# Performance work log

Measured on AMD Instinct MI355X. Metric: run time of the kernel, lower is better.

The kernel has to match this reference:

```python
import jax, jax.numpy as jnp
import numpy as np

LEVEL = 8
THRESHOLD = 0.1
INV_SQRT2 = 0.7071067811865476  # 1/sqrt(2), db1 (Haar) filter coefficient

# Static frequency-order permutation: pywt get_level(order='freq') places the
# natural-order (path-lex: aa,ad,da,dd,...) node n at frequency position gray(n).
_g = np.arange(2 ** LEVEL)
_FREQ_PERM = np.argsort(_g ^ (_g >> 1))  # freq[j] = natural[_FREQ_PERM[j]]


def setup_inputs() -> dict:
    key = jax.random.key(0)
    x = jax.random.normal(key, (128, 65536), dtype=jnp.float32)
    return {"x": x}


def _wavelet_packet_leaves(x):
    """Full db1 wavelet-packet tree to LEVEL; returns [B, 2^L, T/2^L] in freq order.

    For Haar with even-length inputs, pywt's symmetric extension is a no-op:
    a[k] = (x[2k]+x[2k+1])/sqrt2, d[k] = (x[2k]-x[2k+1])/sqrt2.
    """
    B, T = x.shape
    c = x[:, None, :]  # [B, nodes=1, len=T]
    for _ in range(LEVEL):
        ev = c[..., 0::2]
        od = c[..., 1::2]
        a = (ev + od) * INV_SQRT2
        d = (ev - od) * INV_SQRT2
        # interleave children (a,d) adjacent -> natural (path-lex) node order
        c = jnp.concatenate([a[:, :, None, :], d[:, :, None, :]], axis=2)
        c = c.reshape(B, -1, a.shape[-1])
    return c[:, _FREQ_PERM, :]


def reference(x):
    coeffs = _wavelet_packet_leaves(x)          # [B, 2^L, n]
    p = coeffs * coeffs
    p = p / (jnp.sum(p, axis=-1, keepdims=True) + 1e-8)
    entropy = -jnp.sum(p * jnp.log(p + 1e-8), axis=-1)  # [B, 2^L]
    keep = entropy > THRESHOLD                           # [B, 2^L] bool
    # Original returns per-batch stacks of kept nodes (variable length);
    # jit-friendly equivalent: zero out pruned nodes and return the mask.
    out = jnp.where(keep[..., None], coeffs, jnp.zeros((), coeffs.dtype))
    return out, entropy, keep
```

## Files before the change

kernel.cpp:

```cpp
#include <hip/hip_runtime.h>

static constexpr int BROWS = 128;
static constexpr int T     = 65536;
static constexpr int CL    = 256;
static constexpr int NCH   = 256;
static constexpr int NODES = 256;
static constexpr int KG    = 32;
static constexpr int LSTR  = 257;

__device__ __forceinline__ int freq_pos(int h) {
    unsigned r = __brev((unsigned)h) >> 24;
    return (int)(r ^ (r >> 1));
}

__global__ __launch_bounds__(256) void wht_kernel(const float* __restrict__ x,
                                                  float* __restrict__ coeffs) {
    __shared__ float lds[KG][LSTR];

    const int b    = blockIdx.x >> 3;
    const int kg   = blockIdx.x & 7;
    const int k0   = kg * KG;
    const int lane = threadIdx.x & 63;
    const int wave = threadIdx.x >> 6;

    const float* xb = x + (size_t)b * T;

    #pragma unroll
    for (int c = 0; c < KG / 4; ++c) {
        const int kl = wave * (KG / 4) + c;
        float4 v = *(const float4*)(xb + (size_t)(k0 + kl) * CL + lane * 4);

        float4 w;
        w.x = v.x + v.y; w.y = v.x - v.y;
        w.z = v.z + v.w; w.w = v.z - v.w;
        v.x = w.x + w.z; v.z = w.x - w.z;
        v.y = w.y + w.w; v.w = w.y - w.w;

        #pragma unroll
        for (int s = 0; s < 6; ++s) {
            const int mask = 1 << s;
            float4 o;
            o.x = __shfl_xor(v.x, mask, 64);
            o.y = __shfl_xor(v.y, mask, 64);
            o.z = __shfl_xor(v.z, mask, 64);
            o.w = __shfl_xor(v.w, mask, 64);
            const float sgn = 1.0f - 2.0f * (float)((lane >> s) & 1);
            v.x = fmaf(sgn, v.x, o.x);
            v.y = fmaf(sgn, v.y, o.y);
            v.z = fmaf(sgn, v.z, o.z);
            v.w = fmaf(sgn, v.w, o.w);
        }

        lds[kl][freq_pos(4 * lane + 0)] = v.x * 0.0625f;
        lds[kl][freq_pos(4 * lane + 1)] = v.y * 0.0625f;
        lds[kl][freq_pos(4 * lane + 2)] = v.z * 0.0625f;
        lds[kl][freq_pos(4 * lane + 3)] = v.w * 0.0625f;
    }
    __syncthreads();

    float* ob = coeffs + (size_t)b * T + k0;
    const int kk = (threadIdx.x & 7) * 4;
    const int m0 = threadIdx.x >> 3;
    #pragma unroll
    for (int p = 0; p < 8; ++p) {
        const int m = p * 32 + m0;
        float4 v;
        v.x = lds[kk + 0][m];
        v.y = lds[kk + 1][m];
        v.z = lds[kk + 2][m];
        v.w = lds[kk + 3][m];
        *(float4*)(ob + (size_t)m * NCH + kk) = v;
    }
}

__global__ __launch_bounds__(256) void entropy_kernel(float* __restrict__ coeffs,
                                                      float* __restrict__ entropy,
                                                      float* __restrict__ keep) {
    const int lane = threadIdx.x & 63;
    const int wave = threadIdx.x >> 6;
    const int row  = blockIdx.x * 4 + wave;

    float* cp = coeffs + (size_t)row * NCH;
    float4 v = *(const float4*)(cp + lane * 4);

    float4 sq;
    sq.x = v.x * v.x; sq.y = v.y * v.y;
    sq.z = v.z * v.z; sq.w = v.w * v.w;

    float s = sq.x + sq.y + sq.z + sq.w;
    #pragma unroll
    for (int m = 1; m < 64; m <<= 1) s += __shfl_xor(s, m, 64);

    const float inv = 1.0f / (s + 1e-8f);
    const float p0 = sq.x * inv, p1 = sq.y * inv, p2 = sq.z * inv, p3 = sq.w * inv;
    float t = p0 * logf(p0 + 1e-8f) + p1 * logf(p1 + 1e-8f)
            + p2 * logf(p2 + 1e-8f) + p3 * logf(p3 + 1e-8f);
    #pragma unroll
    for (int m = 1; m < 64; m <<= 1) t += __shfl_xor(t, m, 64);

    const float e  = -t;
    const bool  kp = e > 0.1f;

    if (!kp) {
        *(float4*)(cp + lane * 4) = make_float4(0.f, 0.f, 0.f, 0.f);
    }
    if (lane == 0) {
        entropy[row] = e;
        keep[row]    = kp ? 1.0f : 0.0f;
    }
}

extern "C" void kernel_launch(void* const* d_in, const int* in_sizes, int n_in,
                              void* d_out, int out_size, void* d_ws, size_t ws_size,
                              hipStream_t stream) {
    const float* x = (const float*)d_in[0];

    float* coeffs  = (float*)d_out;
    float* entropy = coeffs + (size_t)BROWS * NODES * NCH;
    float* keepf   = entropy + (size_t)BROWS * NODES;

    wht_kernel<<<dim3(BROWS * (NCH / KG)), dim3(256), 0, stream>>>(x, coeffs);
    entropy_kernel<<<dim3(BROWS * NODES / 4), dim3(256), 0, stream>>>(coeffs, entropy, keepf);
}
```

Before: 92.70 us.

## Fuse entropy partial sums into transform kernel, finalize from workspace partials

The transform kernel now accumulates per-node sums of c^2 and c^2*log(c^2) in registers, reduces them across waves in LDS, and writes per-block partials to the workspace. A small finalize kernel combines the 8 partials per row, computes entropy with the identity H = log S - sum(c^2 log c^2)/S, and zeroes pruned rows. This removes the second full read of the coefficients, and the coefficient stores become nontemporal. In exchange it changes the log epsilon handling (1e-35 inside the log, fast __logf), which may shift entropies slightly, and zeroing pruned rows is done with strided per-thread writes.

```diff
diff --git a/kernel.cpp b/kernel.cpp
--- a/kernel.cpp
+++ b/kernel.cpp
@@ -8,13 +8,16 @@
 static constexpr int KG    = 32;
 static constexpr int LSTR  = 257;
 
+typedef float nfloat4 __attribute__((ext_vector_type(4)));
+
 __device__ __forceinline__ int freq_pos(int h) {
     unsigned r = __brev((unsigned)h) >> 24;
     return (int)(r ^ (r >> 1));
 }
 
 __global__ __launch_bounds__(256) void wht_kernel(const float* __restrict__ x,
-                                                  float* __restrict__ coeffs) {
+                                                  float* __restrict__ coeffs,
+                                                  float* __restrict__ part) {
     __shared__ float lds[KG][LSTR];
 
     const int b    = blockIdx.x >> 3;
@@ -24,6 +27,12 @@
     const int wave = threadIdx.x >> 6;
 
     const float* xb = x + (size_t)b * T;
+
+    int npos[4];
+    #pragma unroll
+    for (int i = 0; i < 4; ++i) npos[i] = freq_pos(4 * lane + i);
+    float regA[4] = {0.f, 0.f, 0.f, 0.f};
+    float regB[4] = {0.f, 0.f, 0.f, 0.f};
 
     #pragma unroll
     for (int c = 0; c < KG / 4; ++c) {
@@ -51,10 +60,14 @@
             v.w = fmaf(sgn, v.w, o.w);
         }
 
-        lds[kl][freq_pos(4 * lane + 0)] = v.x * 0.0625f;
-        lds[kl][freq_pos(4 * lane + 1)] = v.y * 0.0625f;
-        lds[kl][freq_pos(4 * lane + 2)] = v.z * 0.0625f;
-        lds[kl][freq_pos(4 * lane + 3)] = v.w * 0.0625f;
+        float cv[4] = {v.x * 0.0625f, v.y * 0.0625f, v.z * 0.0625f, v.w * 0.0625f};
+        #pragma unroll
+        for (int i = 0; i < 4; ++i) {
+            const float s2 = cv[i] * cv[i];
+            regA[i] += s2;
+            regB[i] += s2 * __logf(s2 + 1e-35f);
+            lds[kl][npos[i]] = cv[i];
+        }
     }
     __syncthreads();
 
@@ -64,49 +77,59 @@
     #pragma unroll
     for (int p = 0; p < 8; ++p) {
         const int m = p * 32 + m0;
-        float4 v;
+        nfloat4 v;
         v.x = lds[kk + 0][m];
         v.y = lds[kk + 1][m];
         v.z = lds[kk + 2][m];
         v.w = lds[kk + 3][m];
-        *(float4*)(ob + (size_t)m * NCH + kk) = v;
+        __builtin_nontemporal_store(v, (nfloat4*)(ob + (size_t)m * NCH + kk));
     }
+    __syncthreads();
+
+    float* pl = &lds[0][0];
+    #pragma unroll
+    for (int i = 0; i < 4; ++i) {
+        pl[wave * 512 + npos[i]]       = regA[i];
+        pl[wave * 512 + 256 + npos[i]] = regB[i];
+    }
+    __syncthreads();
+
+    const int n = threadIdx.x;
+    const float A = pl[n] + pl[512 + n] + pl[1024 + n] + pl[1536 + n];
+    const float B = pl[256 + n] + pl[768 + n] + pl[1280 + n] + pl[1792 + n];
+    float* pp = part + (size_t)blockIdx.x * 512;
+    pp[n]       = A;
+    pp[256 + n] = B;
 }
 
-__global__ __launch_bounds__(256) void entropy_kernel(float* __restrict__ coeffs,
-                                                      float* __restrict__ entropy,
-                                                      float* __restrict__ keep) {
-    const int lane = threadIdx.x & 63;
-    const int wave = threadIdx.x >> 6;
-    const int row  = blockIdx.x * 4 + wave;
+__global__ __launch_bounds__(256) void finalize_kernel(const float* __restrict__ part,
+                                                       float* __restrict__ coeffs,
+                                                       float* __restrict__ entropy,
+                                                       float* __restrict__ keep) {
+    const int row = blockIdx.x * 256 + threadIdx.x;
+    const int b = row >> 8;
+    const int n = row & 255;
 
-    float* cp = coeffs + (size_t)row * NCH;
-    float4 v = *(const float4*)(cp + lane * 4);
+    float A = 0.f, B = 0.f;
+    #pragma unroll
+    for (int g = 0; g < 8; ++g) {
+        const float* p = part + (size_t)(b * 8 + g) * 512;
+        A += p[n];
+        B += p[256 + n];
+    }
 
-    float4 sq;
-    sq.x = v.x * v.x; sq.y = v.y * v.y;
-    sq.z = v.z * v.z; sq.w = v.w * v.w;
+    const float S = A + 1e-8f;
+    const float e = (A * __logf(S) - B) / S;
+    const bool kp = e > 0.1f;
 
-    float s = sq.x + sq.y + sq.z + sq.w;
-    #pragma unroll
-    for (int m = 1; m < 64; m <<= 1) s += __shfl_xor(s, m, 64);
-
-    const float inv = 1.0f / (s + 1e-8f);
-    const float p0 = sq.x * inv, p1 = sq.y * inv, p2 = sq.z * inv, p3 = sq.w * inv;
-    float t = p0 * logf(p0 + 1e-8f) + p1 * logf(p1 + 1e-8f)
-            + p2 * logf(p2 + 1e-8f) + p3 * logf(p3 + 1e-8f);
-    #pragma unroll
-    for (int m = 1; m < 64; m <<= 1) t += __shfl_xor(t, m, 64);
-
-    const float e  = -t;
-    const bool  kp = e > 0.1f;
+    entropy[row] = e;
+    keep[row]    = kp ? 1.0f : 0.0f;
 
     if (!kp) {
-        *(float4*)(cp + lane * 4) = make_float4(0.f, 0.f, 0.f, 0.f);
-    }
-    if (lane == 0) {
-        entropy[row] = e;
-        keep[row]    = kp ? 1.0f : 0.0f;
+        float4 z = make_float4(0.f, 0.f, 0.f, 0.f);
+        float4* cp = (float4*)(coeffs + (size_t)row * NCH);
+        #pragma unroll
+        for (int j = 0; j < NCH / 4; ++j) cp[j] = z;
     }
 }
 
@@ -119,6 +142,8 @@
     float* entropy = coeffs + (size_t)BROWS * NODES * NCH;
     float* keepf   = entropy + (size_t)BROWS * NODES;
 
-    wht_kernel<<<dim3(BROWS * (NCH / KG)), dim3(256), 0, stream>>>(x, coeffs);
-    entropy_kernel<<<dim3(BROWS * NODES / 4), dim3(256), 0, stream>>>(coeffs, entropy, keepf);
+    float* part = (float*)d_ws;
+
+    wht_kernel<<<dim3(BROWS * (NCH / KG)), dim3(256), 0, stream>>>(x, coeffs, part);
+    finalize_kernel<<<dim3(BROWS * NODES / 256), dim3(256), 0, stream>>>(part, coeffs, entropy, keepf);
 }
```

Result: faster. 88.41 us (-4.6%).
